# Performance work log

Measured on AMD Instinct MI355X. Metric: run time of the kernel, lower is better.

Reference implementation:

```python
import jax, jax.numpy as jnp
import numpy as np

NNZ = 3355443          # int(4096*4096*(1-0.8))
IN_FEATURES = 4096
OUT_FEATURES = 4096
BATCH = 64
ACTIVE_THRESHOLD = 0.01


def setup_inputs() -> dict:
    key = jax.random.key(0)
    k1, k2, k3, k4 = jax.random.split(key, 4)
    x = jax.random.uniform(k1, (BATCH, IN_FEATURES), dtype=jnp.float32)
    row_indices = jax.random.randint(k2, (NNZ,), 0, OUT_FEATURES, dtype=jnp.int32)
    col_indices = jax.random.randint(k3, (NNZ,), 0, IN_FEATURES, dtype=jnp.int32)
    values = jax.random.normal(k4, (NNZ,), dtype=jnp.float32)
    bias = jnp.zeros((OUT_FEATURES,), dtype=jnp.float32)
    return {"x": x, "row_indices": row_indices, "col_indices": col_indices,
            "values": values, "bias": bias}


def reference(x, row_indices, col_indices, values, bias):
    # Event-driven gating: only columns with x > threshold contribute.
    # Equivalent to masking x, then a standard COO spmv per batch row.
    xm = jnp.where(x > ACTIVE_THRESHOLD, x, jnp.zeros((), x.dtype))   # [B, in]
    contrib = values[None, :] * xm[:, col_indices]                    # [B, nnz]
    out = jnp.zeros((x.shape[0], bias.shape[0]), dtype=x.dtype)
    out = out.at[:, row_indices].add(contrib)                         # scatter-add over rows
    return out + bias[None, :]
```

## Files before the change

### kernel.cpp

```cpp
#include <hip/hip_runtime.h>
#include <hip/hip_bf16.h>
#include <stdint.h>

#define IN_F 4096
#define OUT_F 4096
#define NBKT 256
#define SBLOCKS 410
#define REC_PER_SB 8192
#define SMAX 14336u
#define THRESH 0.01f

typedef unsigned int u32;
typedef unsigned short u16;
typedef __attribute__((ext_vector_type(8))) short short8;
typedef __attribute__((ext_vector_type(4))) float f32x4;

static const size_t WS_XB = 0;
static const size_t WS_OFFA = 524288;
static const size_t WS_SORT = 950272;
static const size_t WS_NEEDED = WS_SORT + (size_t)SBLOCKS * REC_PER_SB * 4;

static __device__ __forceinline__ u16 f2bf(float v) {
  __hip_bfloat16 h = __float2bfloat16(v);
  return *reinterpret_cast<u16*>(&h);
}

__global__ __launch_bounds__(256) void k_xb(const float* __restrict__ x, u16* __restrict__ xB) {
  const int tid = blockIdx.x * 256 + threadIdx.x;
  const int b = tid & 63;
  const int kg = tid >> 6;
  const float* src = x + (size_t)b * IN_F + kg * 8;
  const f32x4 a0 = *reinterpret_cast<const f32x4*>(src);
  const f32x4 a1 = *reinterpret_cast<const f32x4*>(src + 4);
  short8 o;
#pragma unroll
  for (int e = 0; e < 4; ++e) {
    float v = a0[e]; v = (v > THRESH) ? v : 0.0f; o[e] = (short)f2bf(v);
  }
#pragma unroll
  for (int e = 0; e < 4; ++e) {
    float v = a1[e]; v = (v > THRESH) ? v : 0.0f; o[4 + e] = (short)f2bf(v);
  }
  *reinterpret_cast<short8*>(xB + ((size_t)kg * 64 + b) * 8) = o;
}

__global__ __launch_bounds__(1024) void k_scatter(const int* __restrict__ rows,
                                                  const int* __restrict__ cols,
                                                  const float* __restrict__ vals, u32 nnz,
                                                  u32* __restrict__ offA,
                                                  u32* __restrict__ sortg) {
  __shared__ u32 cnt[NBKT];
  __shared__ u32 pref[NBKT + 1];
  __shared__ u32 srt[REC_PER_SB];
  const int tid = threadIdx.x;
  const int lane = tid & 63;
  const int wid = tid >> 6;
  if (tid < NBKT) cnt[tid] = 0;
  __syncthreads();
  const u32 base = blockIdx.x * (u32)REC_PER_SB;
  u32 rec[8], bkt[8], rk[8];
#pragma unroll
  for (int j = 0; j < 8; ++j) {
    const u32 i = base + (u32)j * 1024u + tid;
    bkt[j] = 0xffffffffu;
    if (i < nnz) {
      const u32 r = (u32)rows[i] & 4095u;
      const u32 c = (u32)cols[i] & 4095u;
      rec[j] = (c << 20) | ((r & 15u) << 16) | (u32)f2bf(vals[i]);
      bkt[j] = r >> 4;
      rk[j] = atomicAdd(&cnt[bkt[j]], 1u);
    }
  }
  __syncthreads();
  if (wid == 0) {
    u32 a[4]; u32 s = 0;
#pragma unroll
    for (int j = 0; j < 4; ++j) { a[j] = cnt[lane * 4 + j]; s += a[j]; }
    u32 x = s;
#pragma unroll
    for (int d = 1; d < 64; d <<= 1) {
      const u32 y = (u32)__shfl_up((int)x, d, 64);
      if (lane >= d) x += y;
    }
    u32 e = x - s;
#pragma unroll
    for (int j = 0; j < 4; ++j) { pref[lane * 4 + j] = e; e += a[j]; }
    if (lane == 63) pref[256] = e;
  }
  __syncthreads();
#pragma unroll
  for (int j = 0; j < 8; ++j)
    if (bkt[j] != 0xffffffffu) srt[pref[bkt[j]] + rk[j]] = rec[j];
  if (tid < NBKT + 1) offA[(size_t)blockIdx.x * (NBKT + 1) + tid] = pref[tid];
  __syncthreads();
  u32* dst = sortg + (size_t)blockIdx.x * REC_PER_SB;
#pragma unroll
  for (int j = 0; j < 2; ++j) {
    const int o = j * 4096 + tid * 4;
    const uint4 v = *reinterpret_cast<uint4*>(&srt[o]);
    *reinterpret_cast<uint4*>(&dst[o]) = v;
  }
}

__global__ __launch_bounds__(1024) void k_accum(const u32* __restrict__ sortg,
                                                const u32* __restrict__ offA,
                                                const u16* __restrict__ xB,
                                                const float* __restrict__ bias,
                                                float* __restrict__ out) {
  __shared__ float W[16 * 1024];
  __shared__ u32 S[SMAX];
  __shared__ u32 Gs[412], Gl[412], GP[418];
  const int tid = threadIdx.x;
  const int lane = tid & 63;
  const int w = tid >> 6;
  const u32 t = blockIdx.x;

  if (tid < SBLOCKS) {
    const u32 a = offA[(size_t)tid * (NBKT + 1) + t];
    const u32 b = offA[(size_t)tid * (NBKT + 1) + t + 1];
    Gs[tid] = (u32)tid * REC_PER_SB + a;
    Gl[tid] = b - a;
  } else if (tid < 412) { Gs[tid] = 0; Gl[tid] = 0; }
  __syncthreads();
  if (w == 0) {
    u32 l[7]; u32 s = 0;
#pragma unroll
    for (int j = 0; j < 7; ++j) { const int idx = lane * 7 + j; l[j] = (idx < 412) ? Gl[idx] : 0; s += l[j]; }
    u32 x = s;
#pragma unroll
    for (int d = 1; d < 64; d <<= 1) {
      const u32 y = (u32)__shfl_up((int)x, d, 64);
      if (lane >= d) x += y;
    }
    u32 e = x - s;
#pragma unroll
    for (int j = 0; j < 7; ++j) { const int idx = lane * 7 + j; if (idx < 418) GP[idx] = e; e += l[j]; }
  }
  __syncthreads();
  u32 n = GP[SBLOCKS];
  if (n > SMAX) n = SMAX;
  for (int g = w; g < SBLOCKS; g += 16) {
    const u32 len = Gl[g], src = Gs[g], dst = GP[g];
    for (u32 k = (u32)lane; k < len; k += 64u) {
      const u32 d2 = dst + k;
      if (d2 < SMAX) S[d2] = sortg[src + k];
    }
  }
  __syncthreads();
  u32 rec[14];
#pragma unroll
  for (int j = 0; j < 14; ++j) {
    const u32 i = (u32)j * 1024u + tid;
    rec[j] = (i < n) ? S[i] : 0u;
  }

  f32x4 acc0 = {0.f, 0.f, 0.f, 0.f}, acc1 = {0.f, 0.f, 0.f, 0.f};
  f32x4 acc2 = {0.f, 0.f, 0.f, 0.f}, acc3 = {0.f, 0.f, 0.f, 0.f};
  const int row = lane & 15;
  const int e8 = (lane >> 4) * 8;

  for (int q = 0; q < 4; ++q) {
    __syncthreads();
    const f32x4 z = {0.f, 0.f, 0.f, 0.f};
#pragma unroll
    for (int j = 0; j < 4; ++j)
      *reinterpret_cast<f32x4*>(&W[j * 4096 + tid * 4]) = z;
    __syncthreads();
#pragma unroll
    for (int j = 0; j < 14; ++j) {
      const u32 i = (u32)j * 1024u + tid;
      if (i < n) {
        const u32 rc = rec[j];
        const u32 c = rc >> 20;
        if ((int)(c >> 10) == q) {
          const u32 rl = (rc >> 16) & 15u;
          const u32 cl = (c & 1023u) ^ ((rl & 7u) << 3);
          __hip_atomic_fetch_add(&W[rl * 1024u + cl], __uint_as_float(rc << 16),
                                 __ATOMIC_RELAXED, __HIP_MEMORY_SCOPE_WORKGROUP);
        }
      }
    }
    __syncthreads();
#pragma unroll
    for (int s = 0; s < 2; ++s) {
      const int klb = w * 64 + s * 32 + e8;
      const int sw = klb ^ ((row & 7) << 3);
      const f32x4 wa = *reinterpret_cast<const f32x4*>(&W[row * 1024 + sw]);
      const f32x4 wb = *reinterpret_cast<const f32x4*>(&W[row * 1024 + (sw + 4)]);
      short8 af;
#pragma unroll
      for (int e = 0; e < 4; ++e) af[e] = (short)f2bf(wa[e]);
#pragma unroll
      for (int e = 0; e < 4; ++e) af[4 + e] = (short)f2bf(wb[e]);
      const int kabs = q * 1024 + klb;
      const u16* bp = xB + (size_t)(kabs >> 3) * 512 + (u32)(lane & 15) * 8;
      const short8 b0 = *reinterpret_cast<const short8*>(bp);
      const short8 b1 = *reinterpret_cast<const short8*>(bp + 128);
      const short8 b2 = *reinterpret_cast<const short8*>(bp + 256);
      const short8 b3 = *reinterpret_cast<const short8*>(bp + 384);
      acc0 = __builtin_amdgcn_mfma_f32_16x16x32_bf16(af, b0, acc0, 0, 0, 0);
      acc1 = __builtin_amdgcn_mfma_f32_16x16x32_bf16(af, b1, acc1, 0, 0, 0);
      acc2 = __builtin_amdgcn_mfma_f32_16x16x32_bf16(af, b2, acc2, 0, 0, 0);
      acc3 = __builtin_amdgcn_mfma_f32_16x16x32_bf16(af, b3, acc3, 0, 0, 0);
    }
  }
  __syncthreads();
  {
    const int ccol = lane & 15;
    const int rb = (lane >> 4) * 4;
#pragma unroll
    for (int qq = 0; qq < 4; ++qq) W[((w * 4 + 0) * 16 + rb + qq) * 16 + ccol] = acc0[qq];
#pragma unroll
    for (int qq = 0; qq < 4; ++qq) W[((w * 4 + 1) * 16 + rb + qq) * 16 + ccol] = acc1[qq];
#pragma unroll
    for (int qq = 0; qq < 4; ++qq) W[((w * 4 + 2) * 16 + rb + qq) * 16 + ccol] = acc2[qq];
#pragma unroll
    for (int qq = 0; qq < 4; ++qq) W[((w * 4 + 3) * 16 + rb + qq) * 16 + ccol] = acc3[qq];
  }
  __syncthreads();
  const int rl = tid & 15;
  const int b = tid >> 4;
  float sum = bias[t * 16u + rl];
#pragma unroll
  for (int w2 = 0; w2 < 16; ++w2)
    sum += W[((w2 * 4 + (b >> 4)) * 16 + rl) * 16 + (b & 15)];
  out[(size_t)b * OUT_F + t * 16u + rl] = sum;
}

__global__ __launch_bounds__(256) void k_bias_init(const float* __restrict__ bias,
                                                   float* __restrict__ out) {
  const int i = blockIdx.x * 256 + threadIdx.x;
  if (i < 64 * OUT_F) out[i] = bias[i & (OUT_F - 1)];
}

__global__ __launch_bounds__(256) void k_fallback(const int* __restrict__ rows,
                                                  const int* __restrict__ cols,
                                                  const float* __restrict__ vals,
                                                  const float* __restrict__ x,
                                                  float* __restrict__ out, int nnz) {
  const int gw = (int)(((u32)blockIdx.x * blockDim.x + threadIdx.x) >> 6);
  const int lane = threadIdx.x & 63;
  const int nw = (int)(((u32)gridDim.x * blockDim.x) >> 6);
  for (int i = gw; i < nnz; i += nw) {
    const int r = rows[i];
    const int c = cols[i];
    const float v = vals[i];
    const float xv = x[lane * IN_F + c];
    if (xv > THRESH) atomicAdd(&out[(size_t)lane * OUT_F + r], v * xv);
  }
}

extern "C" void kernel_launch(void* const* d_in, const int* in_sizes, int n_in,
                              void* d_out, int out_size, void* d_ws, size_t ws_size,
                              hipStream_t stream) {
  const float* x = (const float*)d_in[0];
  const int* rows = (const int*)d_in[1];
  const int* cols = (const int*)d_in[2];
  const float* vals = (const float*)d_in[3];
  const float* bias = (const float*)d_in[4];
  float* out = (float*)d_out;
  const int nnz = in_sizes[1];

  if (ws_size >= WS_NEEDED && nnz <= SBLOCKS * REC_PER_SB) {
    u16* xB = (u16*)((char*)d_ws + WS_XB);
    u32* offA = (u32*)((char*)d_ws + WS_OFFA);
    u32* sortg = (u32*)((char*)d_ws + WS_SORT);
    k_xb<<<128, 256, 0, stream>>>(x, xB);
    k_scatter<<<SBLOCKS, 1024, 0, stream>>>(rows, cols, vals, (u32)nnz, offA, sortg);
    k_accum<<<NBKT, 1024, 0, stream>>>(sortg, offA, xB, bias, out);
  } else {
    k_bias_init<<<(64 * OUT_F + 255) / 256, 256, 0, stream>>>(bias, out);
    k_fallback<<<4096, 256, 0, stream>>>(rows, cols, vals, x, out, nnz);
  }
}
```

Baseline: 60.23 us.

## Bin records into per-quarter LDS queues instead of staging and rescanning per pass

Replaces the prefix-scan plus flat LDS staging of bucket records with a direct gather that uses wave-aggregated atomics to append each record into one of four per-column-quarter LDS queues. Each of the four accumulation passes then walks only its own queue instead of rescanning all 14 register-held records per thread and filtering by quarter. This removes a scan, a barrier and redundant predicate work, and adds launch_bounds min-blocks of 1. The cost is LDS atomics on the queue counters, and records beyond a per-quarter capacity are dropped, so a skewed bucket could produce wrong output.

Result: slower. 73.77 us (+22.5%).

```diff
diff --git a/kernel.cpp b/kernel.cpp
--- a/kernel.cpp
+++ b/kernel.cpp
@@ -7,7 +7,7 @@
 #define NBKT 256
 #define SBLOCKS 410
 #define REC_PER_SB 8192
-#define SMAX 14336u
+#define QCAP 3968u
 #define THRESH 0.01f
 
 typedef unsigned int u32;
@@ -102,14 +102,15 @@
   }
 }
 
-__global__ __launch_bounds__(1024) void k_accum(const u32* __restrict__ sortg,
-                                                const u32* __restrict__ offA,
-                                                const u16* __restrict__ xB,
-                                                const float* __restrict__ bias,
-                                                float* __restrict__ out) {
+__global__ __launch_bounds__(1024, 1) void k_accum(const u32* __restrict__ sortg,
+                                                   const u32* __restrict__ offA,
+                                                   const u16* __restrict__ xB,
+                                                   const float* __restrict__ bias,
+                                                   float* __restrict__ out) {
   __shared__ float W[16 * 1024];
-  __shared__ u32 S[SMAX];
-  __shared__ u32 Gs[412], Gl[412], GP[418];
+  __shared__ u32 Q[4][QCAP];
+  __shared__ u32 Gs[SBLOCKS], Gl[SBLOCKS];
+  __shared__ u32 qcur[4];
   const int tid = threadIdx.x;
   const int lane = tid & 63;
   const int w = tid >> 6;
@@ -120,38 +121,49 @@
     const u32 b = offA[(size_t)tid * (NBKT + 1) + t + 1];
     Gs[tid] = (u32)tid * REC_PER_SB + a;
     Gl[tid] = b - a;
-  } else if (tid < 412) { Gs[tid] = 0; Gl[tid] = 0; }
-  __syncthreads();
-  if (w == 0) {
-    u32 l[7]; u32 s = 0;
-#pragma unroll
-    for (int j = 0; j < 7; ++j) { const int idx = lane * 7 + j; l[j] = (idx < 412) ? Gl[idx] : 0; s += l[j]; }
-    u32 x = s;
-#pragma unroll
-    for (int d = 1; d < 64; d <<= 1) {
-      const u32 y = (u32)__shfl_up((int)x, d, 64);
-      if (lane >= d) x += y;
-    }
-    u32 e = x - s;
-#pragma unroll
-    for (int j = 0; j < 7; ++j) { const int idx = lane * 7 + j; if (idx < 418) GP[idx] = e; e += l[j]; }
-  }
-  __syncthreads();
-  u32 n = GP[SBLOCKS];
-  if (n > SMAX) n = SMAX;
-  for (int g = w; g < SBLOCKS; g += 16) {
-    const u32 len = Gl[g], src = Gs[g], dst = GP[g];
-    for (u32 k = (u32)lane; k < len; k += 64u) {
-      const u32 d2 = dst + k;
-      if (d2 < SMAX) S[d2] = sortg[src + k];
-    }
-  }
-  __syncthreads();
-  u32 rec[14];
-#pragma unroll
-  for (int j = 0; j < 14; ++j) {
-    const u32 i = (u32)j * 1024u + tid;
-    rec[j] = (i < n) ? S[i] : 0u;
+  }
+  if (tid < 4) qcur[tid] = 0;
+  __syncthreads();
+
+  for (int ch = 0; ch < 7; ++ch) {
+    u32 rc4[4], ln4[4]; int g4[4];
+#pragma unroll
+    for (int j = 0; j < 4; ++j) {
+      const int idx = ch * 4 + j;
+      g4[j] = w + 16 * idx;
+      ln4[j] = 0; rc4[j] = 0;
+      if (g4[j] < SBLOCKS) {
+        ln4[j] = Gl[g4[j]];
+        if ((u32)lane < ln4[j]) rc4[j] = sortg[Gs[g4[j]] + lane];
+      }
+    }
+#pragma unroll
+    for (int j = 0; j < 4; ++j) {
+      const u32 L = ln4[j];
+      const bool vld = (u32)lane < L;
+      const u32 r = rc4[j];
+      const u32 qv = r >> 30;
+#pragma unroll
+      for (u32 qq = 0; qq < 4; ++qq) {
+        const bool m = vld && (qv == qq);
+        const unsigned long long mask = __ballot(m);
+        if (mask) {
+          const int leader = __builtin_ctzll(mask);
+          u32 bas = 0;
+          if (lane == leader) bas = atomicAdd(&qcur[qq], (u32)__popcll(mask));
+          bas = (u32)__shfl((int)bas, leader, 64);
+          if (m) {
+            const u32 pos = bas + (u32)__popcll(mask & ((1ull << lane) - 1ull));
+            if (pos < QCAP) Q[qq][pos] = r;
+          }
+        }
+      }
+      for (u32 k = 64u + (u32)lane; k < L; k += 64u) {
+        const u32 r2 = sortg[Gs[g4[j]] + k];
+        const u32 pos = atomicAdd(&qcur[r2 >> 30], 1u);
+        if (pos < QCAP) Q[r2 >> 30][pos] = r2;
+      }
+    }
   }
 
   f32x4 acc0 = {0.f, 0.f, 0.f, 0.f}, acc1 = {0.f, 0.f, 0.f, 0.f};
@@ -166,19 +178,13 @@
     for (int j = 0; j < 4; ++j)
       *reinterpret_cast<f32x4*>(&W[j * 4096 + tid * 4]) = z;
     __syncthreads();
-#pragma unroll
-    for (int j = 0; j < 14; ++j) {
-      const u32 i = (u32)j * 1024u + tid;
-      if (i < n) {
-        const u32 rc = rec[j];
-        const u32 c = rc >> 20;
-        if ((int)(c >> 10) == q) {
-          const u32 rl = (rc >> 16) & 15u;
-          const u32 cl = (c & 1023u) ^ ((rl & 7u) << 3);
-          __hip_atomic_fetch_add(&W[rl * 1024u + cl], __uint_as_float(rc << 16),
-                                 __ATOMIC_RELAXED, __HIP_MEMORY_SCOPE_WORKGROUP);
-        }
-      }
+    u32 m = qcur[q]; if (m > QCAP) m = QCAP;
+    for (u32 i = (u32)tid; i < m; i += 1024u) {
+      const u32 rc = Q[q][i];
+      const u32 rl = (rc >> 16) & 15u;
+      const u32 cl = ((rc >> 20) & 1023u) ^ ((rl & 7u) << 3);
+      __hip_atomic_fetch_add(&W[rl * 1024u + cl], __uint_as_float(rc << 16),
+                             __ATOMIC_RELAXED, __HIP_MEMORY_SCOPE_WORKGROUP);
     }
     __syncthreads();
 #pragma unroll
```

## Replace in-accum segmented gather with separate global bin reorder pass

Applied to the files above, without the earlier changes.

The accumulate kernel previously gathered each bucket's records from 410 per-block segments into shared memory. That gather is replaced by two new kernels: a per-bucket prefix scan over the segment counts, and a reorder pass that writes every record into a contiguous global bin per bucket. The scatter kernel now also stores a byte-wide bucket id for each record so the reorder pass can place it. This removes the serialized segment copy and its shared-memory staging from k_accum, at the cost of two extra launches and an extra global round trip over all records.

Measured after the change: 61.87 us. 2.7% more time.

```diff
diff --git a/kernel.cpp b/kernel.cpp
--- a/kernel.cpp
+++ b/kernel.cpp
@@ -12,13 +12,19 @@
 
 typedef unsigned int u32;
 typedef unsigned short u16;
+typedef unsigned char u8;
 typedef __attribute__((ext_vector_type(8))) short short8;
 typedef __attribute__((ext_vector_type(4))) float f32x4;
 
-static const size_t WS_XB = 0;
-static const size_t WS_OFFA = 524288;
-static const size_t WS_SORT = 950272;
-static const size_t WS_NEEDED = WS_SORT + (size_t)SBLOCKS * REC_PER_SB * 4;
+static constexpr size_t pad256(size_t x) { return (x + 255u) & ~(size_t)255u; }
+static constexpr size_t WS_XB    = 0;
+static constexpr size_t WS_OFFA  = pad256(WS_XB + (size_t)512 * 64 * 8 * 2);
+static constexpr size_t WS_SORT  = pad256(WS_OFFA + (size_t)SBLOCKS * (NBKT + 1) * 4);
+static constexpr size_t WS_SORTB = pad256(WS_SORT + (size_t)SBLOCKS * REC_PER_SB * 4);
+static constexpr size_t WS_GOFF  = pad256(WS_SORTB + (size_t)SBLOCKS * REC_PER_SB);
+static constexpr size_t WS_NTOT  = pad256(WS_GOFF + (size_t)NBKT * SBLOCKS * 4);
+static constexpr size_t WS_BINS  = pad256(WS_NTOT + (size_t)NBKT * 4);
+static constexpr size_t WS_NEEDED = WS_BINS + (size_t)NBKT * SMAX * 4;
 
 static __device__ __forceinline__ u16 f2bf(float v) {
   __hip_bfloat16 h = __float2bfloat16(v);
@@ -48,10 +54,12 @@
                                                   const int* __restrict__ cols,
                                                   const float* __restrict__ vals, u32 nnz,
                                                   u32* __restrict__ offA,
-                                                  u32* __restrict__ sortg) {
+                                                  u32* __restrict__ sortg,
+                                                  u8* __restrict__ sortgb) {
   __shared__ u32 cnt[NBKT];
   __shared__ u32 pref[NBKT + 1];
   __shared__ u32 srt[REC_PER_SB];
+  __shared__ __attribute__((aligned(16))) u8 srtb[REC_PER_SB];
   const int tid = threadIdx.x;
   const int lane = tid & 63;
   const int wid = tid >> 6;
@@ -90,68 +98,95 @@
   __syncthreads();
 #pragma unroll
   for (int j = 0; j < 8; ++j)
-    if (bkt[j] != 0xffffffffu) srt[pref[bkt[j]] + rk[j]] = rec[j];
+    if (bkt[j] != 0xffffffffu) {
+      const u32 pos = pref[bkt[j]] + rk[j];
+      srt[pos] = rec[j];
+      srtb[pos] = (u8)bkt[j];
+    }
   if (tid < NBKT + 1) offA[(size_t)blockIdx.x * (NBKT + 1) + tid] = pref[tid];
   __syncthreads();
   u32* dst = sortg + (size_t)blockIdx.x * REC_PER_SB;
 #pragma unroll
   for (int j = 0; j < 2; ++j) {
     const int o = j * 4096 + tid * 4;
-    const uint4 v = *reinterpret_cast<uint4*>(&srt[o]);
-    *reinterpret_cast<uint4*>(&dst[o]) = v;
-  }
-}
-
-__global__ __launch_bounds__(1024) void k_accum(const u32* __restrict__ sortg,
-                                                const u32* __restrict__ offA,
-                                                const u16* __restrict__ xB,
-                                                const float* __restrict__ bias,
-                                                float* __restrict__ out) {
+    *reinterpret_cast<uint4*>(&dst[o]) = *reinterpret_cast<uint4*>(&srt[o]);
+  }
+  if (tid < 512) {
+    uint4* bdst = (uint4*)(sortgb + (size_t)blockIdx.x * REC_PER_SB);
+    bdst[tid] = *reinterpret_cast<uint4*>(&srtb[tid * 16]);
+  }
+}
+
+__global__ __launch_bounds__(512) void k_goff(const u32* __restrict__ offA,
+                                              u32* __restrict__ gOff,
+                                              u32* __restrict__ ntot) {
+  __shared__ u32 wsum[8];
+  const int t = blockIdx.x;
+  const int tid = threadIdx.x;
+  const int lane = tid & 63, w = tid >> 6;
+  u32 v = 0;
+  if (tid < SBLOCKS)
+    v = offA[(size_t)tid * (NBKT + 1) + t + 1] - offA[(size_t)tid * (NBKT + 1) + t];
+  u32 x = v;
+#pragma unroll
+  for (int d = 1; d < 64; d <<= 1) {
+    const u32 y = (u32)__shfl_up((int)x, d, 64);
+    if (lane >= d) x += y;
+  }
+  if (lane == 63) wsum[w] = x;
+  __syncthreads();
+  u32 bse = 0;
+  for (int i = 0; i < w; ++i) bse += wsum[i];
+  const u32 excl = bse + x - v;
+  if (tid < SBLOCKS) gOff[(size_t)t * SBLOCKS + tid] = excl;
+  if (tid == SBLOCKS - 1) ntot[t] = excl + v;
+}
+
+__global__ __launch_bounds__(1024) void k_reorder(const u32* __restrict__ sortg,
+                                                  const u8* __restrict__ sortgb,
+                                                  const u32* __restrict__ offA,
+                                                  const u32* __restrict__ gOff,
+                                                  u32* __restrict__ sortb) {
+  __shared__ u32 pref[NBKT + 1];
+  __shared__ u32 gof[NBKT];
+  const int blk = blockIdx.x;
+  const int tid = threadIdx.x;
+  if (tid < NBKT + 1) pref[tid] = offA[(size_t)blk * (NBKT + 1) + tid];
+  if (tid < NBKT) gof[tid] = gOff[(size_t)tid * SBLOCKS + blk];
+  __syncthreads();
+  const u32 tot = pref[NBKT];
+  const u32* src = sortg + (size_t)blk * REC_PER_SB;
+  const u8* srcb = sortgb + (size_t)blk * REC_PER_SB;
+#pragma unroll
+  for (int j = 0; j < 8; ++j) {
+    const u32 i = (u32)j * 1024u + tid;
+    if (i < tot) {
+      const u32 r = src[i];
+      const u32 t = srcb[i];
+      const u32 d = t * SMAX + gof[t] + (i - pref[t]);
+      sortb[d] = r;
+    }
+  }
+}
+
+__global__ __launch_bounds__(1024, 1) void k_accum(const u32* __restrict__ sortb,
+                                                   const u32* __restrict__ ntot,
+                                                   const u16* __restrict__ xB,
+                                                   const float* __restrict__ bias,
+                                                   float* __restrict__ out) {
   __shared__ float W[16 * 1024];
-  __shared__ u32 S[SMAX];
-  __shared__ u32 Gs[412], Gl[412], GP[418];
   const int tid = threadIdx.x;
   const int lane = tid & 63;
   const int w = tid >> 6;
   const u32 t = blockIdx.x;
-
-  if (tid < SBLOCKS) {
-    const u32 a = offA[(size_t)tid * (NBKT + 1) + t];
-    const u32 b = offA[(size_t)tid * (NBKT + 1) + t + 1];
-    Gs[tid] = (u32)tid * REC_PER_SB + a;
-    Gl[tid] = b - a;
-  } else if (tid < 412) { Gs[tid] = 0; Gl[tid] = 0; }
-  __syncthreads();
-  if (w == 0) {
-    u32 l[7]; u32 s = 0;
-#pragma unroll
-    for (int j = 0; j < 7; ++j) { const int idx = lane * 7 + j; l[j] = (idx < 412) ? Gl[idx] : 0; s += l[j]; }
-    u32 x = s;
-#pragma unroll
-    for (int d = 1; d < 64; d <<= 1) {
-      const u32 y = (u32)__shfl_up((int)x, d, 64);
-      if (lane >= d) x += y;
-    }
-    u32 e = x - s;
-#pragma unroll
-    for (int j = 0; j < 7; ++j) { const int idx = lane * 7 + j; if (idx < 418) GP[idx] = e; e += l[j]; }
-  }
-  __syncthreads();
-  u32 n = GP[SBLOCKS];
+  u32 n = ntot[t];
   if (n > SMAX) n = SMAX;
-  for (int g = w; g < SBLOCKS; g += 16) {
-    const u32 len = Gl[g], src = Gs[g], dst = GP[g];
-    for (u32 k = (u32)lane; k < len; k += 64u) {
-      const u32 d2 = dst + k;
-      if (d2 < SMAX) S[d2] = sortg[src + k];
-    }
-  }
-  __syncthreads();
+  const u32* bin = sortb + (size_t)t * SMAX;
   u32 rec[14];
 #pragma unroll
   for (int j = 0; j < 14; ++j) {
     const u32 i = (u32)j * 1024u + tid;
-    rec[j] = (i < n) ? S[i] : 0u;
+    rec[j] = (i < n) ? bin[i] : 0u;
   }
 
   f32x4 acc0 = {0.f, 0.f, 0.f, 0.f}, acc1 = {0.f, 0.f, 0.f, 0.f};
@@ -171,10 +206,9 @@
       const u32 i = (u32)j * 1024u + tid;
       if (i < n) {
         const u32 rc = rec[j];
-        const u32 c = rc >> 20;
-        if ((int)(c >> 10) == q) {
+        if ((rc >> 30) == (u32)q) {
           const u32 rl = (rc >> 16) & 15u;
-          const u32 cl = (c & 1023u) ^ ((rl & 7u) << 3);
+          const u32 cl = ((rc >> 20) & 1023u) ^ ((rl & 7u) << 3);
           __hip_atomic_fetch_add(&W[rl * 1024u + cl], __uint_as_float(rc << 16),
                                  __ATOMIC_RELAXED, __HIP_MEMORY_SCOPE_WORKGROUP);
         }
@@ -193,7 +227,7 @@
 #pragma unroll
       for (int e = 0; e < 4; ++e) af[4 + e] = (short)f2bf(wb[e]);
       const int kabs = q * 1024 + klb;
-      const u16* bp = xB + (size_t)(kabs >> 3) * 512 + (u32)(lane & 15) * 8;
+      const u16* bp = xB + (size_t)(kabs >> 3) * 512 + (u32)row * 8;
       const short8 b0 = *reinterpret_cast<const short8*>(bp);
       const short8 b1 = *reinterpret_cast<const short8*>(bp + 128);
       const short8 b2 = *reinterpret_cast<const short8*>(bp + 256);
@@ -265,9 +299,15 @@
     u16* xB = (u16*)((char*)d_ws + WS_XB);
     u32* offA = (u32*)((char*)d_ws + WS_OFFA);
     u32* sortg = (u32*)((char*)d_ws + WS_SORT);
+    u8* sortgb = (u8*)((char*)d_ws + WS_SORTB);
+    u32* gOff = (u32*)((char*)d_ws + WS_GOFF);
+    u32* ntot = (u32*)((char*)d_ws + WS_NTOT);
+    u32* sortb = (u32*)((char*)d_ws + WS_BINS);
     k_xb<<<128, 256, 0, stream>>>(x, xB);
-    k_scatter<<<SBLOCKS, 1024, 0, stream>>>(rows, cols, vals, (u32)nnz, offA, sortg);
-    k_accum<<<NBKT, 1024, 0, stream>>>(sortg, offA, xB, bias, out);
+    k_scatter<<<SBLOCKS, 1024, 0, stream>>>(rows, cols, vals, (u32)nnz, offA, sortg, sortgb);
+    k_goff<<<NBKT, 512, 0, stream>>>(offA, gOff, ntot);
+    k_reorder<<<SBLOCKS, 1024, 0, stream>>>(sortg, sortgb, offA, gOff, sortb);
+    k_accum<<<NBKT, 1024, 0, stream>>>(sortb, ntot, xB, bias, out);
   } else {
     k_bias_init<<<(64 * OUT_F + 255) / 256, 256, 0, stream>>>(bias, out);
     k_fallback<<<4096, 256, 0, stream>>>(rows, cols, vals, x, out, nnz);
```
